# Performance work log

Measured on AMD Instinct MI355X. Metric: run time of the kernel, lower is better.

Reference implementation:

```python
import jax, jax.numpy as jnp
import numpy as np
from jax.ops import segment_sum

N = 100_000   # nodes
E = 1_600_000 # edges (avg degree 16)
IN, HID, OUT = 128, 64, 64
NEG_SLOPE = 0.2  # GATConv default negative_slope


def setup_inputs() -> dict:
    key = jax.random.key(0)
    ks = jax.random.split(key, 12)
    def w(k, shape, fan_in):
        return jax.random.normal(k, shape, dtype=jnp.float32) / np.sqrt(fan_in)
    x = jax.random.normal(ks[0], (N, IN), dtype=jnp.float32)
    edge_index = jax.random.randint(ks[1], (2, E), 0, N, dtype=jnp.int64)
    return {
        "x": x,
        "edge_index": edge_index,
        "gcn_w": w(ks[2], (IN, HID), IN),
        "gcn_b": jnp.zeros((HID,), jnp.float32),
        "gat_w": w(ks[3], (HID, HID), HID),
        "att_src": w(ks[4], (HID,), HID),
        "att_dst": w(ks[5], (HID,), HID),
        "gat_b": jnp.zeros((HID,), jnp.float32),
        "sage_wl": w(ks[6], (HID, OUT), HID),
        "sage_wr": w(ks[7], (HID, OUT), HID),
        "sage_b": jnp.zeros((OUT,), jnp.float32),
    }


def _add_self_loops(edge_index):
    loop = jnp.arange(N, dtype=edge_index.dtype)
    src = jnp.concatenate([edge_index[0], loop])
    dst = jnp.concatenate([edge_index[1], loop])
    return src, dst


def _gcn(x, edge_index, w, b):
    # GCNConv: D^{-1/2} (A + I) D^{-1/2} X W + b
    src, dst = _add_self_loops(edge_index)
    h = x @ w                                               # [N, HID]
    deg = segment_sum(jnp.ones_like(dst, jnp.float32), dst, num_segments=N)
    dinv = jnp.where(deg > 0, jax.lax.rsqrt(jnp.maximum(deg, 1.0)), 0.0)
    norm = dinv[src] * dinv[dst]                            # [E+N]
    out = segment_sum(h[src] * norm[:, None], dst, num_segments=N)
    return out + b


def _gat(x, edge_index, w, att_src, att_dst, b):
    # GATConv, heads=1: per-edge softmax over incoming edges of each dst node
    src, dst = _add_self_loops(edge_index)
    h = x @ w                                               # [N, HID]
    a_s = h @ att_src                                       # [N]
    a_d = h @ att_dst                                       # [N]
    e = jax.nn.leaky_relu(a_s[src] + a_d[dst], NEG_SLOPE)   # [E+N]
    # stable segment softmax over dst (every node has a self loop -> nonempty)
    m = jnp.full((N,), -jnp.inf, jnp.float32).at[dst].max(e)
    p = jnp.exp(e - m[dst])
    s = segment_sum(p, dst, num_segments=N)
    alpha = p / s[dst]                                      # [E+N]
    out = segment_sum(h[src] * alpha[:, None], dst, num_segments=N)
    return out + b


def _sage(x, edge_index, wl, wr, b):
    # SAGEConv (mean aggr): W_l * mean_{j in N(i)} x_j + W_r * x_i + b
    src, dst = edge_index[0], edge_index[1]
    ssum = segment_sum(x[src], dst, num_segments=N)         # [N, HID]
    deg = segment_sum(jnp.ones_like(dst, jnp.float32), dst, num_segments=N)
    mean = ssum / jnp.maximum(deg, 1.0)[:, None]
    return mean @ wl + x @ wr + b


def reference(x, edge_index, gcn_w, gcn_b, gat_w, att_src, att_dst, gat_b,
              sage_wl, sage_wr, sage_b):
    h = jax.nn.relu(_gcn(x, edge_index, gcn_w, gcn_b))
    h = jax.nn.relu(_gat(h, edge_index, gat_w, att_src, att_dst, gat_b))
    return _sage(h, edge_index, sage_wl, sage_wr, sage_b)   # [N, OUT]
```

## Files before the change

### kernel.cpp

```cpp
#include <hip/hip_runtime.h>
#include <hip/hip_fp16.h>
#include <math.h>

#define NN 100000
#define NE 1600000
#define INF_ 128
#define HID 64
#define NEG 0.2f
#define NBUK 98
#define ACH 2048

__device__ __forceinline__ float lrelu(float v){ return v > 0.f ? v : NEG*v; }


__global__ void k_zero_i(int* p, int n){
  int i = blockIdx.x*blockDim.x + threadIdx.x;
  if (i < n) p[i] = 0;
}

__global__ __launch_bounds__(256) void kA0(const int* __restrict__ dst,
                                           int* __restrict__ ghist){
  __shared__ int hist[NBUK];
  int t = threadIdx.x;
  if (t < NBUK) hist[t] = 0;
  __syncthreads();
  int eb = blockIdx.x*ACH;
  for (int i = t; i < ACH; i += 256){
    int e = eb + i;
    if (e < NE) atomicAdd(&hist[dst[e] >> 10], 1);
  }
  __syncthreads();
  if (t < NBUK && hist[t]) atomicAdd(&ghist[t], hist[t]);
}

__global__ __launch_bounds__(128) void k_scan_bk(const int* __restrict__ ghist,
                                                 int* __restrict__ bases,
                                                 int* __restrict__ cur,
                                                 int* __restrict__ off){
  __shared__ int l[128];
  int t = threadIdx.x;
  int v = (t < NBUK) ? ghist[t] : 0;
  l[t] = v; __syncthreads();
  for (int o = 1; o < 128; o <<= 1){
    int u = (t >= o) ? l[t-o] : 0;
    __syncthreads();
    l[t] += u;
    __syncthreads();
  }
  if (t < NBUK){ bases[t] = l[t] - v; cur[t] = l[t] - v; }
  if (t == 0){ bases[NBUK] = NE; off[NN] = NE; }
}

__global__ __launch_bounds__(256) void kA1(const int* __restrict__ src,
                                           const int* __restrict__ dst,
                                           int* cur,
                                           unsigned* __restrict__ bucketed){
  __shared__ unsigned pk[ACH];
  __shared__ unsigned char bk[ACH];
  __shared__ int hist[NBUK], base[NBUK];
  int t = threadIdx.x;
  if (t < NBUK) hist[t] = 0;
  __syncthreads();
  int eb = blockIdx.x*ACH;
  for (int i = t; i < ACH; i += 256){
    int e = eb + i;
    if (e < NE){
      int d = dst[e];
      int b = d >> 10;
      atomicAdd(&hist[b], 1);
      pk[i] = ((unsigned)src[e] << 10) | (unsigned)(d & 1023);
      bk[i] = (unsigned char)b;
    } else bk[i] = 0xFF;
  }
  __syncthreads();
  if (t < NBUK){
    base[t] = hist[t] ? atomicAdd(&cur[t], hist[t]) : 0;
    hist[t] = 0;
  }
  __syncthreads();
  for (int i = t; i < ACH; i += 256){
    if (bk[i] != 0xFF){
      int b = bk[i];
      int slot = atomicAdd(&hist[b], 1);
      bucketed[base[b] + slot] = pk[i];
    }
  }
}

__global__ __launch_bounds__(512) void kB(const unsigned* __restrict__ bucketed,
                                          const int* __restrict__ bases,
                                          int* __restrict__ csr,
                                          int* __restrict__ off,
                                          int* __restrict__ cnt,
                                          float* __restrict__ dinv){
  __shared__ int lc[1024];
  __shared__ int lcur[1024];
  __shared__ int red[512];
  int b = blockIdx.x, t = threadIdx.x;
  int bbase = bases[b], bend = bases[b+1];
  lc[t] = 0; lc[t + 512] = 0;
  __syncthreads();
  for (int e = bbase + t; e < bend; e += 512)
    atomicAdd(&lc[bucketed[e] & 1023], 1);
  __syncthreads();
  int a0 = lc[2*t], a1 = lc[2*t+1];
  int s = a0 + a1;
  red[t] = s;
  __syncthreads();
  for (int o = 1; o < 512; o <<= 1){
    int v = (t >= o) ? red[t-o] : 0;
    __syncthreads();
    red[t] += v;
    __syncthreads();
  }
  int e0 = red[t] - s;
  lcur[2*t]   = e0;
  lcur[2*t+1] = e0 + a0;
  int node = b*1024 + 2*t;
  if (node < NN){
    off[node]  = bbase + e0;
    cnt[node]  = a0;
    dinv[node] = rsqrtf((float)a0 + 1.f);
  }
  if (node + 1 < NN){
    off[node+1]  = bbase + e0 + a0;
    cnt[node+1]  = a1;
    dinv[node+1] = rsqrtf((float)a1 + 1.f);
  }
  __syncthreads();
  for (int e = bbase + t; e < bend; e += 512){
    unsigned w = bucketed[e];
    int slot = atomicAdd(&lcur[w & 1023], 1);
    csr[bbase + slot] = (int)(w >> 10);
  }
}


template<int M>
__global__ __launch_bounds__(256, 4) void k_gemm_in(const float* __restrict__ x,
                                                    const float* __restrict__ w,
                                                    const float* __restrict__ dinv,
                                                    float* __restrict__ hs,
                                                    __half* __restrict__ hsH){
  __shared__ float xl[4][8][INF_];
  const int wave = threadIdx.x >> 6, lane = threadIdx.x & 63;
  int rb = blockIdx.x*32 + wave*8;
  if (rb >= NN) return;
  #pragma unroll
  for (int r = 0; r < 8; ++r){
    xl[wave][r][lane]      = x[(size_t)(rb+r)*INF_ + lane];
    xl[wave][r][lane + 64] = x[(size_t)(rb+r)*INF_ + lane + 64];
  }
  float acc[8] = {0.f,0.f,0.f,0.f,0.f,0.f,0.f,0.f};
  #pragma unroll
  for (int c = 0; c < 8; ++c){
    float wv[16];
    #pragma unroll
    for (int j = 0; j < 16; ++j) wv[j] = w[(c*16 + j)*HID + lane];
    #pragma unroll
    for (int r = 0; r < 8; ++r)
      #pragma unroll
      for (int j = 0; j < 16; ++j)
        acc[r] = fmaf(xl[wave][r][c*16 + j], wv[j], acc[r]);
  }
  #pragma unroll
  for (int r = 0; r < 8; ++r){
    float v = acc[r]*dinv[rb+r];
    hs[(size_t)(rb+r)*HID + lane] = v;
    if constexpr (M == 1) hsH[(size_t)(rb+r)*HID + lane] = __float2half(v);
  }
}

template<int M>
__global__ __launch_bounds__(256, 4) void k_gat_lin(const float* __restrict__ h1,
                                                    const float* __restrict__ w,
                                                    const float* __restrict__ atts,
                                                    const float* __restrict__ attd,
                                                    float* __restrict__ h2pre,
                                                    __half* __restrict__ h2preH,
                                                    float* __restrict__ as_,
                                                    float* __restrict__ ad_){
  __shared__ float xl[4][8][HID];
  __shared__ float asl[HID], adl[HID];
  if (threadIdx.x < HID){
    asl[threadIdx.x] = atts[threadIdx.x];
    adl[threadIdx.x] = attd[threadIdx.x];
  }
  __syncthreads();
  const int wave = threadIdx.x >> 6, lane = threadIdx.x & 63;
  int rb = blockIdx.x*32 + wave*8;
  if (rb >= NN) return;
  #pragma unroll
  for (int r = 0; r < 8; ++r)
    xl[wave][r][lane] = h1[(size_t)(rb+r)*HID + lane];
  float acc[8] = {0.f,0.f,0.f,0.f,0.f,0.f,0.f,0.f};
  #pragma unroll
  for (int c = 0; c < 4; ++c){
    float wv[16];
    #pragma unroll
    for (int j = 0; j < 16; ++j) wv[j] = w[(c*16 + j)*HID + lane];
    #pragma unroll
    for (int r = 0; r < 8; ++r)
      #pragma unroll
      for (int j = 0; j < 16; ++j)
        acc[r] = fmaf(xl[wave][r][c*16 + j], wv[j], acc[r]);
  }
  #pragma unroll
  for (int r = 0; r < 8; ++r){
    h2pre[(size_t)(rb+r)*HID + lane] = acc[r];
    if constexpr (M == 1) h2preH[(size_t)(rb+r)*HID + lane] = __float2half(acc[r]);
    xl[wave][r][lane] = acc[r];
  }
  int rr = lane >> 3, t = lane & 7;
  float vs = 0.f, vd = 0.f;
  #pragma unroll
  for (int i = 0; i < 8; ++i){
    float v = xl[wave][rr][t + 8*i];
    vs = fmaf(v, asl[t + 8*i], vs);
    vd = fmaf(v, adl[t + 8*i], vd);
  }
  #pragma unroll
  for (int o = 1; o < 8; o <<= 1){
    vs += __shfl_xor(vs, o, 64);
    vd += __shfl_xor(vd, o, 64);
  }
  if (t == 0){ as_[rb + rr] = vs; ad_[rb + rr] = vd; }
}

__global__ __launch_bounds__(256, 4) void k_sage_dense(const float* mean,
                                                       const float* __restrict__ h2,
                                                       const float* __restrict__ wlh,
                                                       const float* __restrict__ wrh,
                                                       const float* __restrict__ b,
                                                       float* out){
  __shared__ float ml[4][8][HID];
  __shared__ float hl[4][8][HID];
  const int wave = threadIdx.x >> 6, lane = threadIdx.x & 63;
  int rb = blockIdx.x*32 + wave*8;
  if (rb >= NN) return;
  float bl = b[lane];
  #pragma unroll
  for (int r = 0; r < 8; ++r){
    ml[wave][r][lane] = mean[(size_t)(rb+r)*HID + lane];
    hl[wave][r][lane] = h2[(size_t)(rb+r)*HID + lane];
  }
  float acc[8] = {bl,bl,bl,bl,bl,bl,bl,bl};
  #pragma unroll
  for (int c = 0; c < 4; ++c){
    float wvl[16], wvr[16];
    #pragma unroll
    for (int j = 0; j < 16; ++j){
      wvl[j] = wlh[(c*16 + j)*HID + lane];
      wvr[j] = wrh[(c*16 + j)*HID + lane];
    }
    #pragma unroll
    for (int r = 0; r < 8; ++r)
      #pragma unroll
      for (int j = 0; j < 16; ++j){
        acc[r] = fmaf(ml[wave][r][c*16 + j], wvl[j], acc[r]);
        acc[r] = fmaf(hl[wave][r][c*16 + j], wvr[j], acc[r]);
      }
  }
  #pragma unroll
  for (int r = 0; r < 8; ++r)
    out[(size_t)(rb+r)*HID + lane] = acc[r];
}


template<int M>
__device__ __forceinline__ void row_acc(const float4* __restrict__ r4,
                                        const uint2*  __restrict__ rh,
                                        size_t s, int f, float p, float4& acc){
  if constexpr (M == 1){
    uint2 v = rh[s*16 + f];
    half2* ph = (half2*)&v;
    float2 fa = __half22float2(ph[0]);
    float2 fb = __half22float2(ph[1]);
    acc.x = fmaf(fa.x, p, acc.x); acc.y = fmaf(fa.y, p, acc.y);
    acc.z = fmaf(fb.x, p, acc.z); acc.w = fmaf(fb.y, p, acc.w);
  } else {
    float4 r = r4[s*16 + f];
    acc.x = fmaf(r.x, p, acc.x); acc.y = fmaf(r.y, p, acc.y);
    acc.z = fmaf(r.z, p, acc.z); acc.w = fmaf(r.w, p, acc.w);
  }
}

template<int M>
__global__ __launch_bounds__(256) void k_gcn_gather(const int* __restrict__ csr,
                                                    const int* __restrict__ off,
                                                    const float4* __restrict__ hs4,
                                                    const uint2*  __restrict__ hsH,
                                                    const float* __restrict__ dinv,
                                                    const float4* __restrict__ gcn_b4,
                                                    float4* __restrict__ h1_4){
  int node = blockIdx.x*4 + (threadIdx.x >> 6);
  if (node >= NN) return;
  int lane = threadIdx.x & 63;
  int q = lane >> 4, f = lane & 15;
  int beg = off[node], end = off[node+1];
  float4 acc = {0.f,0.f,0.f,0.f};
  for (int c = beg; c < end; c += 64){
    int n = end - c; if (n > 64) n = 64;
    int idx = (lane < n) ? csr[c + lane] : 0;
    for (int k = 0; k < n; k += 16){
      int e0 = k + q, e1 = k + 4 + q, e2 = k + 8 + q, e3 = k + 12 + q;
      int s0 = __shfl(idx, e0, 64);
      int s1 = __shfl(idx, e1, 64);
      int s2 = __shfl(idx, e2, 64);
      int s3 = __shfl(idx, e3, 64);
      if (e0 < n) row_acc<M>(hs4, hsH, (size_t)s0, f, 1.f, acc);
      if (e1 < n) row_acc<M>(hs4, hsH, (size_t)s1, f, 1.f, acc);
      if (e2 < n) row_acc<M>(hs4, hsH, (size_t)s2, f, 1.f, acc);
      if (e3 < n) row_acc<M>(hs4, hsH, (size_t)s3, f, 1.f, acc);
    }
  }
  #pragma unroll
  for (int o = 16; o <= 32; o <<= 1){
    acc.x += __shfl_xor(acc.x, o, 64);
    acc.y += __shfl_xor(acc.y, o, 64);
    acc.z += __shfl_xor(acc.z, o, 64);
    acc.w += __shfl_xor(acc.w, o, 64);
  }
  if (q == 0){
    float4 s  = hs4[(size_t)node*16 + f];
    float  di = dinv[node];
    float4 b4 = gcn_b4[f];
    float4 o;
    o.x = fmaxf((acc.x + s.x)*di + b4.x, 0.f);
    o.y = fmaxf((acc.y + s.y)*di + b4.y, 0.f);
    o.z = fmaxf((acc.z + s.z)*di + b4.z, 0.f);
    o.w = fmaxf((acc.w + s.w)*di + b4.w, 0.f);
    h1_4[(size_t)node*16 + f] = o;
  }
}

template<int M>
__global__ __launch_bounds__(256) void k_gat_gather(const int* __restrict__ csr,
                                                    const int* __restrict__ off,
                                                    const float* __restrict__ as_,
                                                    const float* __restrict__ ad_,
                                                    const float4* __restrict__ h2pre4,
                                                    const uint2*  __restrict__ h2preH,
                                                    const float4* __restrict__ gat_b4,
                                                    float4* __restrict__ h2_4,
                                                    uint2* __restrict__ h2H){
  int node = blockIdx.x*4 + (threadIdx.x >> 6);
  if (node >= NN) return;
  int lane = threadIdx.x & 63;
  int q = lane >> 4, f = lane & 15;
  int beg = off[node], end = off[node+1];
  float adi = ad_[node];
  float ps = expf(fminf(lrelu(as_[node] + adi), 80.f));
  float ssum = 0.f;
  float4 acc = {0.f,0.f,0.f,0.f};
  for (int c = beg; c < end; c += 64){
    int n = end - c; if (n > 64) n = 64;
    int idx = 0; float pv = 0.f;
    if (lane < n){
      idx = csr[c + lane];
      pv = expf(fminf(lrelu(as_[idx] + adi), 80.f));
    }
    for (int k = 0; k < n; k += 16){
      int e0 = k + q, e1 = k + 4 + q, e2 = k + 8 + q, e3 = k + 12 + q;
      int s0 = __shfl(idx, e0, 64); float p0 = __shfl(pv, e0, 64);
      int s1 = __shfl(idx, e1, 64); float p1 = __shfl(pv, e1, 64);
      int s2 = __shfl(idx, e2, 64); float p2 = __shfl(pv, e2, 64);
      int s3 = __shfl(idx, e3, 64); float p3 = __shfl(pv, e3, 64);
      if (e0 < n){ row_acc<M>(h2pre4, h2preH, (size_t)s0, f, p0, acc); ssum += p0; }
      if (e1 < n){ row_acc<M>(h2pre4, h2preH, (size_t)s1, f, p1, acc); ssum += p1; }
      if (e2 < n){ row_acc<M>(h2pre4, h2preH, (size_t)s2, f, p2, acc); ssum += p2; }
      if (e3 < n){ row_acc<M>(h2pre4, h2preH, (size_t)s3, f, p3, acc); ssum += p3; }
    }
  }
  #pragma unroll
  for (int o = 16; o <= 32; o <<= 1){
    acc.x += __shfl_xor(acc.x, o, 64);
    acc.y += __shfl_xor(acc.y, o, 64);
    acc.z += __shfl_xor(acc.z, o, 64);
    acc.w += __shfl_xor(acc.w, o, 64);
    ssum  += __shfl_xor(ssum,  o, 64);
  }
  if (q == 0){
    float inv = 1.f/(ssum + ps);
    float4 h0 = h2pre4[(size_t)node*16 + f];
    float4 b4 = gat_b4[f];
    float4 o;
    o.x = fmaxf((acc.x + h0.x*ps)*inv + b4.x, 0.f);
    o.y = fmaxf((acc.y + h0.y*ps)*inv + b4.y, 0.f);
    o.z = fmaxf((acc.z + h0.z*ps)*inv + b4.z, 0.f);
    o.w = fmaxf((acc.w + h0.w*ps)*inv + b4.w, 0.f);
    h2_4[(size_t)node*16 + f] = o;
    if constexpr (M == 1){
      union { half2 h[2]; uint2 u; } pk;
      pk.h[0] = __floats2half2_rn(o.x, o.y);
      pk.h[1] = __floats2half2_rn(o.z, o.w);
      h2H[(size_t)node*16 + f] = pk.u;
    }
  }
}

template<int M>
__global__ __launch_bounds__(256) void k_sage_gather(const int* __restrict__ csr,
                                                     const int* __restrict__ off,
                                                     const int* __restrict__ cnt,
                                                     const float4* __restrict__ h2_4,
                                                     const uint2*  __restrict__ h2H,
                                                     float4* __restrict__ mean4){
  int node = blockIdx.x*4 + (threadIdx.x >> 6);
  if (node >= NN) return;
  int lane = threadIdx.x & 63;
  int q = lane >> 4, f = lane & 15;
  int beg = off[node], end = off[node+1];
  float4 acc = {0.f,0.f,0.f,0.f};
  for (int c = beg; c < end; c += 64){
    int n = end - c; if (n > 64) n = 64;
    int idx = (lane < n) ? csr[c + lane] : 0;
    for (int k = 0; k < n; k += 16){
      int e0 = k + q, e1 = k + 4 + q, e2 = k + 8 + q, e3 = k + 12 + q;
      int s0 = __shfl(idx, e0, 64);
      int s1 = __shfl(idx, e1, 64);
      int s2 = __shfl(idx, e2, 64);
      int s3 = __shfl(idx, e3, 64);
      if (e0 < n) row_acc<M>(h2_4, h2H, (size_t)s0, f, 1.f, acc);
      if (e1 < n) row_acc<M>(h2_4, h2H, (size_t)s1, f, 1.f, acc);
      if (e2 < n) row_acc<M>(h2_4, h2H, (size_t)s2, f, 1.f, acc);
      if (e3 < n) row_acc<M>(h2_4, h2H, (size_t)s3, f, 1.f, acc);
    }
  }
  #pragma unroll
  for (int o = 16; o <= 32; o <<= 1){
    acc.x += __shfl_xor(acc.x, o, 64);
    acc.y += __shfl_xor(acc.y, o, 64);
    acc.z += __shfl_xor(acc.z, o, 64);
    acc.w += __shfl_xor(acc.w, o, 64);
  }
  if (q == 0){
    float inv = 1.f/fmaxf((float)cnt[node], 1.f);
    float4 o = {acc.x*inv, acc.y*inv, acc.z*inv, acc.w*inv};
    mean4[(size_t)node*16 + f] = o;
  }
}


extern "C" void kernel_launch(void* const* d_in, const int* in_sizes, int n_in,
                              void* d_out, int out_size, void* d_ws, size_t ws_size,
                              hipStream_t stream) {
  const float* x      = (const float*)d_in[0];
  const int*   ei     = (const int*)d_in[1];
  const int*   src    = ei;
  const int*   dstp   = ei + NE;
  const float* gcn_w  = (const float*)d_in[2];
  const float* gcn_b  = (const float*)d_in[3];
  const float* gat_w  = (const float*)d_in[4];
  const float* att_s  = (const float*)d_in[5];
  const float* att_d  = (const float*)d_in[6];
  const float* gat_b  = (const float*)d_in[7];
  const float* s_wl   = (const float*)d_in[8];
  const float* s_wr   = (const float*)d_in[9];
  const float* s_b    = (const float*)d_in[10];
  float* outp = (float*)d_out;

  int*   ghist = (int*)d_ws;
  int*   bases = ghist + 128;
  int*   cur   = bases + 128;
  int*   cnt   = cur + 128;
  int*   off   = cnt + NN;
  float* dinv  = (float*)(off + NN + 8);
  float* as_   = dinv + NN;
  float* ad_   = as_  + NN;
  unsigned* bucketed = (unsigned*)(ad_ + NN);
  int*   csr   = (int*)(bucketed + NE);
  float* BIG0  = (float*)(csr + NE);
  float* BIG1  = BIG0 + (size_t)NN*HID;

  size_t base_words = 384 + (size_t)5*NN + 8 + (size_t)2*NE;
  size_t need2 = (base_words + (size_t)2*NN*HID)*4;

  const size_t NH = (size_t)NN*HID;
  const int B = 256;
  const int GROWS = (NN + 31)/32;
  const int GG = (NN + 3)/4;
  const int GA = (NE + ACH - 1)/ACH;

  k_zero_i <<<1, 128, 0, stream>>>(ghist, NBUK);
  kA0      <<<GA, B, 0, stream>>>(dstp, ghist);
  k_scan_bk<<<1, 128, 0, stream>>>(ghist, bases, cur, off);
  kA1      <<<GA, B, 0, stream>>>(src, dstp, cur, bucketed);
  kB       <<<NBUK, 512, 0, stream>>>(bucketed, bases, csr, off, cnt, dinv);

  if (ws_size >= need2){
    float* P_hs    = BIG0;
    float* P_h1    = BIG1;
    float* P_h2pre = BIG0;
    float* P_h2    = BIG1;
    float* P_mean  = BIG0;
    __half* HS_H    = (__half*)outp;
    __half* H2PRE_H = (__half*)outp + NH;
    __half* H2_H    = (__half*)outp;

    k_gemm_in<1><<<GROWS, B, 0, stream>>>(x, gcn_w, dinv, P_hs, HS_H);
    k_gcn_gather<1><<<GG, B, 0, stream>>>(csr, off, (const float4*)P_hs,
        (const uint2*)HS_H, dinv, (const float4*)gcn_b, (float4*)P_h1);

    k_gat_lin<1><<<GROWS, B, 0, stream>>>(P_h1, gat_w, att_s, att_d,
        P_h2pre, H2PRE_H, as_, ad_);
    k_gat_gather<1><<<GG, B, 0, stream>>>(csr, off, as_, ad_,
        (const float4*)P_h2pre, (const uint2*)H2PRE_H, (const float4*)gat_b,
        (float4*)P_h2, (uint2*)H2_H);

    k_sage_gather<1><<<GG, B, 0, stream>>>(csr, off, cnt,
        (const float4*)P_h2, (const uint2*)H2_H, (float4*)P_mean);
    k_sage_dense<<<GROWS, B, 0, stream>>>(P_mean, P_h2, s_wl, s_wr, s_b, outp);
  } else {
    float* P_hs    = outp;
    float* P_h1    = BIG0;
    float* P_h2pre = outp;
    float* P_h2    = BIG0;
    float* P_mean  = outp;

    k_gemm_in<0><<<GROWS, B, 0, stream>>>(x, gcn_w, dinv, P_hs, nullptr);
    k_gcn_gather<0><<<GG, B, 0, stream>>>(csr, off, (const float4*)P_hs,
        nullptr, dinv, (const float4*)gcn_b, (float4*)P_h1);
    k_gat_lin<0><<<GROWS, B, 0, stream>>>(P_h1, gat_w, att_s, att_d,
        P_h2pre, nullptr, as_, ad_);
    k_gat_gather<0><<<GG, B, 0, stream>>>(csr, off, as_, ad_,
        (const float4*)P_h2pre, nullptr, (const float4*)gat_b, (float4*)P_h2, nullptr);
    k_sage_gather<0><<<GG, B, 0, stream>>>(csr, off, cnt,
        (const float4*)P_h2, nullptr, (float4*)P_mean);
    k_sage_dense<<<GROWS, B, 0, stream>>>(P_mean, P_h2, s_wl, s_wr, s_b, outp);
  }
}
```

Before: 320.5 us.

## Process two nodes per wave in gathers and halve CSR bucket size

Each of the three gather kernels now has one wavefront handle two destination nodes at once. It interleaves their neighbor index loads and row accumulations, which doubles the memory-level parallelism per wave and evens out degree imbalance. The CSR build uses 512-node buckets instead of 1024, giving twice as many blocks for the sort kernel and more parallelism there. The risk is wasted lanes when the two nodes have very different degrees, plus higher register pressure. The launch grid assumes NN is divisible by 8, with no bounds guard.

```diff
diff --git a/kernel.cpp b/kernel.cpp
--- a/kernel.cpp
+++ b/kernel.cpp
@@ -7,7 +7,7 @@
 #define INF_ 128
 #define HID 64
 #define NEG 0.2f
-#define NBUK 98
+#define NBUK 196
 #define ACH 2048
 
 __device__ __forceinline__ float lrelu(float v){ return v > 0.f ? v : NEG*v; }
@@ -27,21 +27,21 @@
   int eb = blockIdx.x*ACH;
   for (int i = t; i < ACH; i += 256){
     int e = eb + i;
-    if (e < NE) atomicAdd(&hist[dst[e] >> 10], 1);
+    if (e < NE) atomicAdd(&hist[dst[e] >> 9], 1);
   }
   __syncthreads();
   if (t < NBUK && hist[t]) atomicAdd(&ghist[t], hist[t]);
 }
 
-__global__ __launch_bounds__(128) void k_scan_bk(const int* __restrict__ ghist,
+__global__ __launch_bounds__(256) void k_scan_bk(const int* __restrict__ ghist,
                                                  int* __restrict__ bases,
                                                  int* __restrict__ cur,
                                                  int* __restrict__ off){
-  __shared__ int l[128];
+  __shared__ int l[256];
   int t = threadIdx.x;
   int v = (t < NBUK) ? ghist[t] : 0;
   l[t] = v; __syncthreads();
-  for (int o = 1; o < 128; o <<= 1){
+  for (int o = 1; o < 256; o <<= 1){
     int u = (t >= o) ? l[t-o] : 0;
     __syncthreads();
     l[t] += u;
@@ -66,9 +66,9 @@
     int e = eb + i;
     if (e < NE){
       int d = dst[e];
-      int b = d >> 10;
+      int b = d >> 9;
       atomicAdd(&hist[b], 1);
-      pk[i] = ((unsigned)src[e] << 10) | (unsigned)(d & 1023);
+      pk[i] = ((unsigned)src[e] << 9) | (unsigned)(d & 511);
       bk[i] = (unsigned char)b;
     } else bk[i] = 0xFF;
   }
@@ -87,27 +87,27 @@
   }
 }
 
-__global__ __launch_bounds__(512) void kB(const unsigned* __restrict__ bucketed,
+__global__ __launch_bounds__(256) void kB(const unsigned* __restrict__ bucketed,
                                           const int* __restrict__ bases,
                                           int* __restrict__ csr,
                                           int* __restrict__ off,
                                           int* __restrict__ cnt,
                                           float* __restrict__ dinv){
-  __shared__ int lc[1024];
-  __shared__ int lcur[1024];
-  __shared__ int red[512];
+  __shared__ int lc[512];
+  __shared__ int lcur[512];
+  __shared__ int red[256];
   int b = blockIdx.x, t = threadIdx.x;
   int bbase = bases[b], bend = bases[b+1];
-  lc[t] = 0; lc[t + 512] = 0;
-  __syncthreads();
-  for (int e = bbase + t; e < bend; e += 512)
-    atomicAdd(&lc[bucketed[e] & 1023], 1);
+  lc[t] = 0; lc[t + 256] = 0;
+  __syncthreads();
+  for (int e = bbase + t; e < bend; e += 256)
+    atomicAdd(&lc[bucketed[e] & 511], 1);
   __syncthreads();
   int a0 = lc[2*t], a1 = lc[2*t+1];
   int s = a0 + a1;
   red[t] = s;
   __syncthreads();
-  for (int o = 1; o < 512; o <<= 1){
+  for (int o = 1; o < 256; o <<= 1){
     int v = (t >= o) ? red[t-o] : 0;
     __syncthreads();
     red[t] += v;
@@ -116,7 +116,7 @@
   int e0 = red[t] - s;
   lcur[2*t]   = e0;
   lcur[2*t+1] = e0 + a0;
-  int node = b*1024 + 2*t;
+  int node = b*512 + 2*t;
   if (node < NN){
     off[node]  = bbase + e0;
     cnt[node]  = a0;
@@ -128,10 +128,10 @@
     dinv[node+1] = rsqrtf((float)a1 + 1.f);
   }
   __syncthreads();
-  for (int e = bbase + t; e < bend; e += 512){
+  for (int e = bbase + t; e < bend; e += 256){
     unsigned w = bucketed[e];
-    int slot = atomicAdd(&lcur[w & 1023], 1);
-    csr[bbase + slot] = (int)(w >> 10);
+    int slot = atomicAdd(&lcur[w & 511], 1);
+    csr[bbase + slot] = (int)(w >> 9);
   }
 }
 
@@ -293,43 +293,54 @@
                                                     const float* __restrict__ dinv,
                                                     const float4* __restrict__ gcn_b4,
                                                     float4* __restrict__ h1_4){
-  int node = blockIdx.x*4 + (threadIdx.x >> 6);
-  if (node >= NN) return;
-  int lane = threadIdx.x & 63;
+  const int wave = threadIdx.x >> 6, lane = threadIdx.x & 63;
+  int n0 = blockIdx.x*8 + wave*2, n1 = n0 + 1;
   int q = lane >> 4, f = lane & 15;
-  int beg = off[node], end = off[node+1];
-  float4 acc = {0.f,0.f,0.f,0.f};
-  for (int c = beg; c < end; c += 64){
-    int n = end - c; if (n > 64) n = 64;
-    int idx = (lane < n) ? csr[c + lane] : 0;
-    for (int k = 0; k < n; k += 16){
-      int e0 = k + q, e1 = k + 4 + q, e2 = k + 8 + q, e3 = k + 12 + q;
-      int s0 = __shfl(idx, e0, 64);
-      int s1 = __shfl(idx, e1, 64);
-      int s2 = __shfl(idx, e2, 64);
-      int s3 = __shfl(idx, e3, 64);
-      if (e0 < n) row_acc<M>(hs4, hsH, (size_t)s0, f, 1.f, acc);
-      if (e1 < n) row_acc<M>(hs4, hsH, (size_t)s1, f, 1.f, acc);
-      if (e2 < n) row_acc<M>(hs4, hsH, (size_t)s2, f, 1.f, acc);
-      if (e3 < n) row_acc<M>(hs4, hsH, (size_t)s3, f, 1.f, acc);
+  int b0 = off[n0], e0_ = off[n0+1];
+  int b1 = e0_,     e1_ = off[n0+2];
+  float4 A0 = {0,0,0,0}, A1 = {0,0,0,0};
+  int c0 = b0, c1 = b1;
+  while (c0 < e0_ || c1 < e1_){
+    int m0 = e0_ - c0; if (m0 > 64) m0 = 64;
+    int m1 = e1_ - c1; if (m1 > 64) m1 = 64;
+    int i0 = (lane < m0) ? csr[c0 + lane] : 0;
+    int i1 = (lane < m1) ? csr[c1 + lane] : 0;
+    int mm = m0 > m1 ? m0 : m1;
+    for (int k = 0; k < mm; k += 16){
+      int ka = k + q, kb = k + 4 + q, kc = k + 8 + q, kd = k + 12 + q;
+      int s0a = __shfl(i0, ka, 64), s1a = __shfl(i1, ka, 64);
+      int s0b = __shfl(i0, kb, 64), s1b = __shfl(i1, kb, 64);
+      int s0c = __shfl(i0, kc, 64), s1c = __shfl(i1, kc, 64);
+      int s0d = __shfl(i0, kd, 64), s1d = __shfl(i1, kd, 64);
+      if (ka < m0) row_acc<M>(hs4, hsH, (size_t)s0a, f, 1.f, A0);
+      if (ka < m1) row_acc<M>(hs4, hsH, (size_t)s1a, f, 1.f, A1);
+      if (kb < m0) row_acc<M>(hs4, hsH, (size_t)s0b, f, 1.f, A0);
+      if (kb < m1) row_acc<M>(hs4, hsH, (size_t)s1b, f, 1.f, A1);
+      if (kc < m0) row_acc<M>(hs4, hsH, (size_t)s0c, f, 1.f, A0);
+      if (kc < m1) row_acc<M>(hs4, hsH, (size_t)s1c, f, 1.f, A1);
+      if (kd < m0) row_acc<M>(hs4, hsH, (size_t)s0d, f, 1.f, A0);
+      if (kd < m1) row_acc<M>(hs4, hsH, (size_t)s1d, f, 1.f, A1);
     }
+    c0 += 64; c1 += 64;
   }
   #pragma unroll
   for (int o = 16; o <= 32; o <<= 1){
-    acc.x += __shfl_xor(acc.x, o, 64);
-    acc.y += __shfl_xor(acc.y, o, 64);
-    acc.z += __shfl_xor(acc.z, o, 64);
-    acc.w += __shfl_xor(acc.w, o, 64);
-  }
-  if (q == 0){
+    A0.x += __shfl_xor(A0.x, o, 64); A1.x += __shfl_xor(A1.x, o, 64);
+    A0.y += __shfl_xor(A0.y, o, 64); A1.y += __shfl_xor(A1.y, o, 64);
+    A0.z += __shfl_xor(A0.z, o, 64); A1.z += __shfl_xor(A1.z, o, 64);
+    A0.w += __shfl_xor(A0.w, o, 64); A1.w += __shfl_xor(A1.w, o, 64);
+  }
+  if (q < 2){
+    int node = q ? n1 : n0;
+    float4 A = q ? A1 : A0;
     float4 s  = hs4[(size_t)node*16 + f];
     float  di = dinv[node];
     float4 b4 = gcn_b4[f];
     float4 o;
-    o.x = fmaxf((acc.x + s.x)*di + b4.x, 0.f);
-    o.y = fmaxf((acc.y + s.y)*di + b4.y, 0.f);
-    o.z = fmaxf((acc.z + s.z)*di + b4.z, 0.f);
-    o.w = fmaxf((acc.w + s.w)*di + b4.w, 0.f);
+    o.x = fmaxf((A.x + s.x)*di + b4.x, 0.f);
+    o.y = fmaxf((A.y + s.y)*di + b4.y, 0.f);
+    o.z = fmaxf((A.z + s.z)*di + b4.z, 0.f);
+    o.w = fmaxf((A.w + s.w)*di + b4.w, 0.f);
     h1_4[(size_t)node*16 + f] = o;
   }
 }
@@ -344,51 +355,65 @@
                                                     const float4* __restrict__ gat_b4,
                                                     float4* __restrict__ h2_4,
                                                     uint2* __restrict__ h2H){
-  int node = blockIdx.x*4 + (threadIdx.x >> 6);
-  if (node >= NN) return;
-  int lane = threadIdx.x & 63;
+  const int wave = threadIdx.x >> 6, lane = threadIdx.x & 63;
+  int n0 = blockIdx.x*8 + wave*2, n1 = n0 + 1;
   int q = lane >> 4, f = lane & 15;
-  int beg = off[node], end = off[node+1];
-  float adi = ad_[node];
-  float ps = expf(fminf(lrelu(as_[node] + adi), 80.f));
-  float ssum = 0.f;
-  float4 acc = {0.f,0.f,0.f,0.f};
-  for (int c = beg; c < end; c += 64){
-    int n = end - c; if (n > 64) n = 64;
-    int idx = 0; float pv = 0.f;
-    if (lane < n){
-      idx = csr[c + lane];
-      pv = expf(fminf(lrelu(as_[idx] + adi), 80.f));
+  int b0 = off[n0], e0_ = off[n0+1];
+  int b1 = e0_,     e1_ = off[n0+2];
+  float adi0 = ad_[n0], adi1 = ad_[n1];
+  float ps0 = expf(fminf(lrelu(as_[n0] + adi0), 80.f));
+  float ps1 = expf(fminf(lrelu(as_[n1] + adi1), 80.f));
+  float S0 = 0.f, S1 = 0.f;
+  float4 A0 = {0,0,0,0}, A1 = {0,0,0,0};
+  int c0 = b0, c1 = b1;
+  while (c0 < e0_ || c1 < e1_){
+    int m0 = e0_ - c0; if (m0 > 64) m0 = 64;
+    int m1 = e1_ - c1; if (m1 > 64) m1 = 64;
+    int i0 = 0, i1 = 0; float p0 = 0.f, p1 = 0.f;
+    if (lane < m0){ i0 = csr[c0 + lane]; p0 = expf(fminf(lrelu(as_[i0] + adi0), 80.f)); }
+    if (lane < m1){ i1 = csr[c1 + lane]; p1 = expf(fminf(lrelu(as_[i1] + adi1), 80.f)); }
+    int mm = m0 > m1 ? m0 : m1;
+    for (int k = 0; k < mm; k += 16){
+      int ka = k + q, kb = k + 4 + q, kc = k + 8 + q, kd = k + 12 + q;
+      int s0a = __shfl(i0, ka, 64); float w0a = __shfl(p0, ka, 64);
+      int s1a = __shfl(i1, ka, 64); float w1a = __shfl(p1, ka, 64);
+      int s0b = __shfl(i0, kb, 64); float w0b = __shfl(p0, kb, 64);
+      int s1b = __shfl(i1, kb, 64); float w1b = __shfl(p1, kb, 64);
+      int s0c = __shfl(i0, kc, 64); float w0c = __shfl(p0, kc, 64);
+      int s1c = __shfl(i1, kc, 64); float w1c = __shfl(p1, kc, 64);
+      int s0d = __shfl(i0, kd, 64); float w0d = __shfl(p0, kd, 64);
+      int s1d = __shfl(i1, kd, 64); float w1d = __shfl(p1, kd, 64);
+      if (ka < m0){ row_acc<M>(h2pre4, h2preH, (size_t)s0a, f, w0a, A0); S0 += w0a; }
+      if (ka < m1){ row_acc<M>(h2pre4, h2preH, (size_t)s1a, f, w1a, A1); S1 += w1a; }
+      if (kb < m0){ row_acc<M>(h2pre4, h2preH, (size_t)s0b, f, w0b, A0); S0 += w0b; }
+      if (kb < m1){ row_acc<M>(h2pre4, h2preH, (size_t)s1b, f, w1b, A1); S1 += w1b; }
+      if (kc < m0){ row_acc<M>(h2pre4, h2preH, (size_t)s0c, f, w0c, A0); S0 += w0c; }
+      if (kc < m1){ row_acc<M>(h2pre4, h2preH, (size_t)s1c, f, w1c, A1); S1 += w1c; }
+      if (kd < m0){ row_acc<M>(h2pre4, h2preH, (size_t)s0d, f, w0d, A0); S0 += w0d; }
+      if (kd < m1){ row_acc<M>(h2pre4, h2preH, (size_t)s1d, f, w1d, A1); S1 += w1d; }
     }
-    for (int k = 0; k < n; k += 16){
-      int e0 = k + q, e1 = k + 4 + q, e2 = k + 8 + q, e3 = k + 12 + q;
-      int s0 = __shfl(idx, e0, 64); float p0 = __shfl(pv, e0, 64);
-      int s1 = __shfl(idx, e1, 64); float p1 = __shfl(pv, e1, 64);
-      int s2 = __shfl(idx, e2, 64); float p2 = __shfl(pv, e2, 64);
-      int s3 = __shfl(idx, e3, 64); float p3 = __shfl(pv, e3, 64);
-      if (e0 < n){ row_acc<M>(h2pre4, h2preH, (size_t)s0, f, p0, acc); ssum += p0; }
-      if (e1 < n){ row_acc<M>(h2pre4, h2preH, (size_t)s1, f, p1, acc); ssum += p1; }
-      if (e2 < n){ row_acc<M>(h2pre4, h2preH, (size_t)s2, f, p2, acc); ssum += p2; }
-      if (e3 < n){ row_acc<M>(h2pre4, h2preH, (size_t)s3, f, p3, acc); ssum += p3; }
-    }
+    c0 += 64; c1 += 64;
   }
   #pragma unroll
   for (int o = 16; o <= 32; o <<= 1){
-    acc.x += __shfl_xor(acc.x, o, 64);
-    acc.y += __shfl_xor(acc.y, o, 64);
-    acc.z += __shfl_xor(acc.z, o, 64);
-    acc.w += __shfl_xor(acc.w, o, 64);
-    ssum  += __shfl_xor(ssum,  o, 64);
-  }
-  if (q == 0){
-    float inv = 1.f/(ssum + ps);
+    A0.x += __shfl_xor(A0.x, o, 64); A1.x += __shfl_xor(A1.x, o, 64);
+    A0.y += __shfl_xor(A0.y, o, 64); A1.y += __shfl_xor(A1.y, o, 64);
+    A0.z += __shfl_xor(A0.z, o, 64); A1.z += __shfl_xor(A1.z, o, 64);
+    A0.w += __shfl_xor(A0.w, o, 64); A1.w += __shfl_xor(A1.w, o, 64);
+    S0   += __shfl_xor(S0,   o, 64); S1   += __shfl_xor(S1,   o, 64);
+  }
+  if (q < 2){
+    int node = q ? n1 : n0;
+    float4 A = q ? A1 : A0;
+    float ps = q ? ps1 : ps0;
+    float inv = 1.f/((q ? S1 : S0) + ps);
     float4 h0 = h2pre4[(size_t)node*16 + f];
     float4 b4 = gat_b4[f];
     float4 o;
-    o.x = fmaxf((acc.x + h0.x*ps)*inv + b4.x, 0.f);
-    o.y = fmaxf((acc.y + h0.y*ps)*inv + b4.y, 0.f);
-    o.z = fmaxf((acc.z + h0.z*ps)*inv + b4.z, 0.f);
-    o.w = fmaxf((acc.w + h0.w*ps)*inv + b4.w, 0.f);
+    o.x = fmaxf((A.x + h0.x*ps)*inv + b4.x, 0.f);
+    o.y = fmaxf((A.y + h0.y*ps)*inv + b4.y, 0.f);
+    o.z = fmaxf((A.z + h0.z*ps)*inv + b4.z, 0.f);
+    o.w = fmaxf((A.w + h0.w*ps)*inv + b4.w, 0.f);
     h2_4[(size_t)node*16 + f] = o;
     if constexpr (M == 1){
       union { half2 h[2]; uint2 u; } pk;
@@ -406,37 +431,48 @@
                                                      const float4* __restrict__ h2_4,
                                                      const uint2*  __restrict__ h2H,
                                                      float4* __restrict__ mean4){
-  int node = blockIdx.x*4 + (threadIdx.x >> 6);
-  if (node >= NN) return;
-  int lane = threadIdx.x & 63;
+  const int wave = threadIdx.x >> 6, lane = threadIdx.x & 63;
+  int n0 = blockIdx.x*8 + wave*2, n1 = n0 + 1;
   int q = lane >> 4, f = lane & 15;
-  int beg = off[node], end = off[node+1];
-  float4 acc = {0.f,0.f,0.f,0.f};
-  for (int c = beg; c < end; c += 64){
-    int n = end - c; if (n > 64) n = 64;
-    int idx = (lane < n) ? csr[c + lane] : 0;
-    for (int k = 0; k < n; k += 16){
-      int e0 = k + q, e1 = k + 4 + q, e2 = k + 8 + q, e3 = k + 12 + q;
-      int s0 = __shfl(idx, e0, 64);
-      int s1 = __shfl(idx, e1, 64);
-      int s2 = __shfl(idx, e2, 64);
-      int s3 = __shfl(idx, e3, 64);
-      if (e0 < n) row_acc<M>(h2_4, h2H, (size_t)s0, f, 1.f, acc);
-      if (e1 < n) row_acc<M>(h2_4, h2H, (size_t)s1, f, 1.f, acc);
-      if (e2 < n) row_acc<M>(h2_4, h2H, (size_t)s2, f, 1.f, acc);
-      if (e3 < n) row_acc<M>(h2_4, h2H, (size_t)s3, f, 1.f, acc);
+  int b0 = off[n0], e0_ = off[n0+1];
+  int b1 = e0_,     e1_ = off[n0+2];
+  float4 A0 = {0,0,0,0}, A1 = {0,0,0,0};
+  int c0 = b0, c1 = b1;
+  while (c0 < e0_ || c1 < e1_){
+    int m0 = e0_ - c0; if (m0 > 64) m0 = 64;
+    int m1 = e1_ - c1; if (m1 > 64) m1 = 64;
+    int i0 = (lane < m0) ? csr[c0 + lane] : 0;
+    int i1 = (lane < m1) ? csr[c1 + lane] : 0;
+    int mm = m0 > m1 ? m0 : m1;
+    for (int k = 0; k < mm; k += 16){
+      int ka = k + q, kb = k + 4 + q, kc = k + 8 + q, kd = k + 12 + q;
+      int s0a = __shfl(i0, ka, 64), s1a = __shfl(i1, ka, 64);
+      int s0b = __shfl(i0, kb, 64), s1b = __shfl(i1, kb, 64);
+      int s0c = __shfl(i0, kc, 64), s1c = __shfl(i1, kc, 64);
+      int s0d = __shfl(i0, kd, 64), s1d = __shfl(i1, kd, 64);
+      if (ka < m0) row_acc<M>(h2_4, h2H, (size_t)s0a, f, 1.f, A0);
+      if (ka < m1) row_acc<M>(h2_4, h2H, (size_t)s1a, f, 1.f, A1);
+      if (kb < m0) row_acc<M>(h2_4, h2H, (size_t)s0b, f, 1.f, A0);
+      if (kb < m1) row_acc<M>(h2_4, h2H, (size_t)s1b, f, 1.f, A1);
+      if (kc < m0) row_acc<M>(h2_4, h2H, (size_t)s0c, f, 1.f, A0);
+      if (kc < m1) row_acc<M>(h2_4, h2H, (size_t)s1c, f, 1.f, A1);
+      if (kd < m0) row_acc<M>(h2_4, h2H, (size_t)s0d, f, 1.f, A0);
+      if (kd < m1) row_acc<M>(h2_4, h2H, (size_t)s1d, f, 1.f, A1);
     }
+    c0 += 64; c1 += 64;
   }
   #pragma unroll
   for (int o = 16; o <= 32; o <<= 1){
-    acc.x += __shfl_xor(acc.x, o, 64);
-    acc.y += __shfl_xor(acc.y, o, 64);
-    acc.z += __shfl_xor(acc.z, o, 64);
-    acc.w += __shfl_xor(acc.w, o, 64);
-  }
-  if (q == 0){
+    A0.x += __shfl_xor(A0.x, o, 64); A1.x += __shfl_xor(A1.x, o, 64);
+    A0.y += __shfl_xor(A0.y, o, 64); A1.y += __shfl_xor(A1.y, o, 64);
+    A0.z += __shfl_xor(A0.z, o, 64); A1.z += __shfl_xor(A1.z, o, 64);
+    A0.w += __shfl_xor(A0.w, o, 64); A1.w += __shfl_xor(A1.w, o, 64);
+  }
+  if (q < 2){
+    int node = q ? n1 : n0;
+    float4 A = q ? A1 : A0;
     float inv = 1.f/fmaxf((float)cnt[node], 1.f);
-    float4 o = {acc.x*inv, acc.y*inv, acc.z*inv, acc.w*inv};
+    float4 o = {A.x*inv, A.y*inv, A.z*inv, A.w*inv};
     mean4[(size_t)node*16 + f] = o;
   }
 }
@@ -461,9 +497,9 @@
   float* outp = (float*)d_out;
 
   int*   ghist = (int*)d_ws;
-  int*   bases = ghist + 128;
-  int*   cur   = bases + 128;
-  int*   cnt   = cur + 128;
+  int*   bases = ghist + 256;
+  int*   cur   = bases + 256;
+  int*   cnt   = cur + 256;
   int*   off   = cnt + NN;
   float* dinv  = (float*)(off + NN + 8);
   float* as_   = dinv + NN;
@@ -473,20 +509,20 @@
   float* BIG0  = (float*)(csr + NE);
   float* BIG1  = BIG0 + (size_t)NN*HID;
 
-  size_t base_words = 384 + (size_t)5*NN + 8 + (size_t)2*NE;
+  size_t base_words = 768 + (size_t)5*NN + 8 + (size_t)2*NE;
   size_t need2 = (base_words + (size_t)2*NN*HID)*4;
 
   const size_t NH = (size_t)NN*HID;
   const int B = 256;
   const int GROWS = (NN + 31)/32;
-  const int GG = (NN + 3)/4;
+  const int GG2 = NN/8;
   const int GA = (NE + ACH - 1)/ACH;
 
-  k_zero_i <<<1, 128, 0, stream>>>(ghist, NBUK);
+  k_zero_i <<<1, 256, 0, stream>>>(ghist, NBUK);
   kA0      <<<GA, B, 0, stream>>>(dstp, ghist);
-  k_scan_bk<<<1, 128, 0, stream>>>(ghist, bases, cur, off);
+  k_scan_bk<<<1, 256, 0, stream>>>(ghist, bases, cur, off);
   kA1      <<<GA, B, 0, stream>>>(src, dstp, cur, bucketed);
-  kB       <<<NBUK, 512, 0, stream>>>(bucketed, bases, csr, off, cnt, dinv);
+  kB       <<<NBUK, 256, 0, stream>>>(bucketed, bases, csr, off, cnt, dinv);
 
   if (ws_size >= need2){
     float* P_hs    = BIG0;
@@ -499,16 +535,16 @@
     __half* H2_H    = (__half*)outp;
 
     k_gemm_in<1><<<GROWS, B, 0, stream>>>(x, gcn_w, dinv, P_hs, HS_H);
-    k_gcn_gather<1><<<GG, B, 0, stream>>>(csr, off, (const float4*)P_hs,
+    k_gcn_gather<1><<<GG2, B, 0, stream>>>(csr, off, (const float4*)P_hs,
         (const uint2*)HS_H, dinv, (const float4*)gcn_b, (float4*)P_h1);
 
     k_gat_lin<1><<<GROWS, B, 0, stream>>>(P_h1, gat_w, att_s, att_d,
         P_h2pre, H2PRE_H, as_, ad_);
-    k_gat_gather<1><<<GG, B, 0, stream>>>(csr, off, as_, ad_,
+    k_gat_gather<1><<<GG2, B, 0, stream>>>(csr, off, as_, ad_,
         (const float4*)P_h2pre, (const uint2*)H2PRE_H, (const float4*)gat_b,
         (float4*)P_h2, (uint2*)H2_H);
 
-    k_sage_gather<1><<<GG, B, 0, stream>>>(csr, off, cnt,
+    k_sage_gather<1><<<GG2, B, 0, stream>>>(csr, off, cnt,
         (const float4*)P_h2, (const uint2*)H2_H, (float4*)P_mean);
     k_sage_dense<<<GROWS, B, 0, stream>>>(P_mean, P_h2, s_wl, s_wr, s_b, outp);
   } else {
@@ -519,13 +555,13 @@
     float* P_mean  = outp;
 
     k_gemm_in<0><<<GROWS, B, 0, stream>>>(x, gcn_w, dinv, P_hs, nullptr);
-    k_gcn_gather<0><<<GG, B, 0, stream>>>(csr, off, (const float4*)P_hs,
+    k_gcn_gather<0><<<GG2, B, 0, stream>>>(csr, off, (const float4*)P_hs,
         nullptr, dinv, (const float4*)gcn_b, (float4*)P_h1);
     k_gat_lin<0><<<GROWS, B, 0, stream>>>(P_h1, gat_w, att_s, att_d,
         P_h2pre, nullptr, as_, ad_);
-    k_gat_gather<0><<<GG, B, 0, stream>>>(csr, off, as_, ad_,
+    k_gat_gather<0><<<GG2, B, 0, stream>>>(csr, off, as_, ad_,
         (const float4*)P_h2pre, nullptr, (const float4*)gat_b, (float4*)P_h2, nullptr);
-    k_sage_gather<0><<<GG, B, 0, stream>>>(csr, off, cnt,
+    k_sage_gather<0><<<GG2, B, 0, stream>>>(csr, off, cnt,
         (const float4*)P_h2, nullptr, (float4*)P_mean);
     k_sage_dense<<<GROWS, B, 0, stream>>>(P_mean, P_h2, s_wl, s_wr, s_b, outp);
   }
```

Measured after the change: 302.4 us. -5.6%, faster.
